# Optimization experiments

Measured on AMD Instinct MI355X. Metric: run time of the kernel, lower is better.

Reference implementation:

```python
import jax, jax.numpy as jnp
import numpy as np

D = 256
FF = 1024
NH = 8
BZ, TL = 8, 1024
L, Hs, Ws = 1, 64, 64


def _linear(x, w, b):
    # torch nn.Linear convention: w is [out, in]
    return x @ w.T + b


def _ln(x, g, b, eps=1e-5):
    m = x.mean(-1, keepdims=True)
    v = ((x - m) ** 2).mean(-1, keepdims=True)
    return (x - m) / jnp.sqrt(v + eps) * g + b


def setup_inputs() -> dict:
    key = jax.random.key(0)
    ks = jax.random.split(key, 16)
    s = 0.02
    inp = {
        "tgt": jax.random.normal(ks[0], (BZ, TL, D), jnp.float32),
        "reference_points": jax.random.uniform(ks[1], (BZ, TL, 2), jnp.float32),
        "srcs": jax.random.normal(ks[2], (BZ, L, D, Hs, Ws), jnp.float32),
        "posemb_2d": jax.random.normal(ks[3], (BZ, TL, D), jnp.float32),
        # self-attn (nn.MultiheadAttention) params
        "in_proj_w": jax.random.normal(ks[4], (3 * D, D), jnp.float32) * s,
        "in_proj_b": jnp.zeros((3 * D,), jnp.float32),
        "out_proj_w": jax.random.normal(ks[5], (D, D), jnp.float32) * s,
        "out_proj_b": jnp.zeros((D,), jnp.float32),
        # hand-rolled cross-attn linears (q, k, v, out)
        "lin_q_w": jax.random.normal(ks[6], (D, D), jnp.float32) * s,
        "lin_q_b": jnp.zeros((D,), jnp.float32),
        "lin_k_w": jax.random.normal(ks[7], (D, D), jnp.float32) * s,
        "lin_k_b": jnp.zeros((D,), jnp.float32),
        "lin_v_w": jax.random.normal(ks[8], (D, D), jnp.float32) * s,
        "lin_v_b": jnp.zeros((D,), jnp.float32),
        "lin_o_w": jax.random.normal(ks[9], (D, D), jnp.float32) * s,
        "lin_o_b": jnp.zeros((D,), jnp.float32),
        # layer norms
        "norm1_g": jnp.ones((D,), jnp.float32),
        "norm1_b": jnp.zeros((D,), jnp.float32),
        "norm2_g": jnp.ones((D,), jnp.float32),
        "norm2_b": jnp.zeros((D,), jnp.float32),
        # FFN
        "ffn_w1": jax.random.normal(ks[10], (FF, D), jnp.float32) * s,
        "ffn_b1": jnp.zeros((FF,), jnp.float32),
        "ffn_w2": jax.random.normal(ks[11], (D, FF), jnp.float32) * s,
        "ffn_b2": jnp.zeros((D,), jnp.float32),
        "ffn_norm_g": jnp.ones((D,), jnp.float32),
        "ffn_norm_b": jnp.zeros((D,), jnp.float32),
    }
    return inp


def reference(tgt, reference_points, srcs, posemb_2d,
              in_proj_w, in_proj_b, out_proj_w, out_proj_b,
              lin_q_w, lin_q_b, lin_k_w, lin_k_b, lin_v_w, lin_v_b,
              lin_o_w, lin_o_b,
              norm1_g, norm1_b, norm2_g, norm2_b,
              ffn_w1, ffn_b1, ffn_w2, ffn_b2, ffn_norm_g, ffn_norm_b):
    bz, tl, c = tgt.shape
    nh = NH
    dh = c // nh
    scale = dh ** -0.5

    # ---- self-attention (nn.MultiheadAttention math) ----
    qk = tgt + posemb_2d  # q = k = with_pos_embed(tgt, posemb_2d_)
    wq, wk, wv = in_proj_w[:c], in_proj_w[c:2 * c], in_proj_w[2 * c:]
    bq, bk, bv = in_proj_b[:c], in_proj_b[c:2 * c], in_proj_b[2 * c:]
    qp = _linear(qk, wq, bq).reshape(bz, tl, nh, dh)
    kp = _linear(qk, wk, bk).reshape(bz, tl, nh, dh)
    vp = _linear(tgt, wv, bv).reshape(bz, tl, nh, dh)
    att = jax.nn.softmax(jnp.einsum('bqhd,bkhd->bhqk', qp * scale, kp), axis=-1)
    sa = jnp.einsum('bhqk,bkhd->bqhd', att, vp).reshape(bz, tl, c)
    sa = _linear(sa, out_proj_w, out_proj_b)
    tgt = _ln(tgt + sa, norm2_g, norm2_b)

    # ---- hand-rolled cross attention ----
    bz_, l, c_, h, w = srcs.shape
    s = jnp.transpose(srcs.reshape(bz_ * l, c_, h, w), (0, 2, 3, 1)).reshape(bz_ * l, h * w, c_)
    query = _linear(tgt, lin_q_w, lin_q_b)          # [bz, tl, c]
    key = _linear(s, lin_k_w, lin_k_b)              # [bz*l, hw, c]
    value = _linear(s, lin_v_w, lin_v_b)
    affinity = jax.nn.softmax(jnp.einsum('bqc,bkc->bqk', query, key), axis=-1)  # no 1/sqrt(d) scale, faithful
    tgt2 = _linear(jnp.einsum('bqk,bkc->bqc', affinity, value), lin_o_w, lin_o_b)
    tgt = _ln(tgt + tgt2, norm1_g, norm1_b)

    # ---- FFN ----
    src2 = _linear(jax.nn.relu(_linear(tgt, ffn_w1, ffn_b1)), ffn_w2, ffn_b2)
    tgt = _ln(tgt + src2, ffn_norm_g, ffn_norm_b)
    return tgt
```

## Files before the change

### kernel.cpp

```cpp
#include <hip/hip_runtime.h>
#include <hip/hip_bf16.h>
#include <math.h>

typedef __attribute__((ext_vector_type(8))) __bf16 bf16x8;
typedef __attribute__((ext_vector_type(4))) __bf16 bf16x4;
typedef __attribute__((ext_vector_type(2))) __bf16 bf16x2;
typedef __attribute__((ext_vector_type(4))) float  f32x4;

#define MFMA16(a,b,c) __builtin_amdgcn_mfma_f32_16x16x32_bf16((a),(b),(c),0,0,0)

__device__ __forceinline__ unsigned pack2bf(float a, float b){
  bf16x2 t; t[0] = (__bf16)a; t[1] = (__bf16)b;
  return __builtin_bit_cast(unsigned, t);
}
__device__ __forceinline__ int perm1(int r){ return ((r<<2)|(r>>1)) & 7; }

template<int BM, bool RELU, int OUTMODE, bool ADD2>
__global__ __launch_bounds__(256) void gemm_bt(
    const float* __restrict__ A, const float* __restrict__ A2,
    const float* __restrict__ W,
    const float* __restrict__ bias, void* __restrict__ Cv,
    int M, int N, int K, int ldc, int coff, float oscale)
{
  constexpr int MT = BM/32;
  __shared__ __align__(16) __bf16 As[BM][40];
  __shared__ __align__(16) __bf16 Bs[64][40];

  const int tid  = threadIdx.x;
  const int wid  = tid >> 6;
  const int lane = tid & 63;
  const int wr   = wid >> 1;
  const int wc   = wid & 1;
  const int lq   = lane & 15;
  const int lk8  = (lane >> 4) << 3;
  const int rb   = (lane >> 4) << 2;

  const int m0 = blockIdx.x * BM;
  const int n0 = blockIdx.y * 64;

  const int scg = (tid & 7) << 2;
  const int sr  = tid >> 3;

  f32x4 acc[MT][2];
  #pragma unroll
  for (int i=0;i<MT;i++)
    #pragma unroll
    for (int j=0;j<2;j++) acc[i][j] = f32x4{0.f,0.f,0.f,0.f};

  for (int k0=0; k0<K; k0+=32){
    __syncthreads();
    #pragma unroll
    for (int i=0;i<MT;i++){
      const int row = sr + i*32;
      float4 a4 = *(const float4*)&A[(size_t)(m0+row)*K + k0 + scg];
      if (ADD2){
        const float4 a42 = *(const float4*)&A2[(size_t)(m0+row)*K + k0 + scg];
        a4.x+=a42.x; a4.y+=a42.y; a4.z+=a42.z; a4.w+=a42.w;
      }
      bf16x4 h; h[0]=(__bf16)a4.x; h[1]=(__bf16)a4.y; h[2]=(__bf16)a4.z; h[3]=(__bf16)a4.w;
      *(bf16x4*)&As[row][scg] = h;
    }
    #pragma unroll
    for (int i=0;i<2;i++){
      const int row = sr + i*32;
      const float4 a4 = *(const float4*)&W[(size_t)(n0+row)*K + k0 + scg];
      bf16x4 h; h[0]=(__bf16)a4.x; h[1]=(__bf16)a4.y; h[2]=(__bf16)a4.z; h[3]=(__bf16)a4.w;
      *(bf16x4*)&Bs[row][scg] = h;
    }
    __syncthreads();
    bf16x8 af[MT], bfr[2];
    #pragma unroll
    for (int i=0;i<MT;i++) af[i]  = *(const bf16x8*)&As[wr*(BM/2) + i*16 + lq][lk8];
    #pragma unroll
    for (int j=0;j<2;j++)  bfr[j] = *(const bf16x8*)&Bs[wc*32 + j*16 + lq][lk8];
    #pragma unroll
    for (int i=0;i<MT;i++)
      #pragma unroll
      for (int j=0;j<2;j++)
        acc[i][j] = MFMA16(af[i], bfr[j], acc[i][j]);
  }

  #pragma unroll
  for (int i=0;i<MT;i++)
    #pragma unroll
    for (int j=0;j<2;j++){
      const int coln = n0 + wc*32 + j*16 + lq;
      const float bv = bias ? bias[coln] : 0.f;
      if (OUTMODE == 2){
        const int rowm0 = m0 + wr*(BM/2) + i*16 + rb;
        bf16x4 hv;
        #pragma unroll
        for (int r=0;r<4;r++){
          float vv = (acc[i][j][r] + bv) * oscale;
          if (RELU) vv = fmaxf(vv, 0.f);
          hv[r] = (__bf16)vv;
        }
        *(bf16x4*)&((__bf16*)Cv)[((size_t)((rowm0>>10)*256) + coln)*1024 + (rowm0&1023)] = hv;
      } else {
        #pragma unroll
        for (int r=0;r<4;r++){
          const int rowm = m0 + wr*(BM/2) + i*16 + rb + r;
          float vv = (acc[i][j][r] + bv) * oscale;
          if (RELU) vv = fmaxf(vv, 0.f);
          const size_t idx = (size_t)rowm*ldc + coff + coln;
          if (OUTMODE == 1) ((__bf16*)Cv)[idx] = (__bf16)vv;
          else              ((float*)Cv)[idx]  = vv;
        }
      }
    }
}

template<bool TRANSOUT>
__global__ __launch_bounds__(256) void gemm_srcs(
    const float* __restrict__ S, const float* __restrict__ W,
    const float* __restrict__ bias, __bf16* __restrict__ C)
{
  __shared__ __align__(16) __bf16 As[128][40];
  __shared__ __align__(16) __bf16 Bs[64][40];

  const int tid  = threadIdx.x;
  const int wid  = tid >> 6;
  const int lane = tid & 63;
  const int wr   = wid >> 1;
  const int wc   = wid & 1;
  const int lq   = lane & 15;
  const int lk8  = (lane >> 4) << 3;
  const int rb   = (lane >> 4) << 2;

  const int m0 = blockIdx.x * 128;
  const int n0 = blockIdx.y * 64;
  const int bb = m0 >> 12;
  const int p0 = m0 & 4095;

  const int cA = tid & 31;
  const int qA = tid >> 5;
  const int scg = (tid & 7) << 2;
  const int sr  = tid >> 3;

  f32x4 acc[4][2];
  #pragma unroll
  for (int i=0;i<4;i++)
    #pragma unroll
    for (int j=0;j<2;j++) acc[i][j] = f32x4{0.f,0.f,0.f,0.f};

  for (int k0=0; k0<256; k0+=32){
    __syncthreads();
    const float* sbase = &S[((size_t)bb*256 + k0 + cA)*4096 + p0];
    #pragma unroll
    for (int ps=0; ps<4; ps++){
      const int p = ps*32 + qA*4;
      const float4 f4 = *(const float4*)(sbase + p);
      As[p+0][cA] = (__bf16)f4.x;
      As[p+1][cA] = (__bf16)f4.y;
      As[p+2][cA] = (__bf16)f4.z;
      As[p+3][cA] = (__bf16)f4.w;
    }
    #pragma unroll
    for (int i=0;i<2;i++){
      const int row = sr + i*32;
      const float4 a4 = *(const float4*)&W[(size_t)(n0+row)*256 + k0 + scg];
      bf16x4 h; h[0]=(__bf16)a4.x; h[1]=(__bf16)a4.y; h[2]=(__bf16)a4.z; h[3]=(__bf16)a4.w;
      *(bf16x4*)&Bs[row][scg] = h;
    }
    __syncthreads();
    bf16x8 af[4], bfr[2];
    #pragma unroll
    for (int i=0;i<4;i++) af[i]  = *(const bf16x8*)&As[wr*64 + i*16 + lq][lk8];
    #pragma unroll
    for (int j=0;j<2;j++) bfr[j] = *(const bf16x8*)&Bs[wc*32 + j*16 + lq][lk8];
    #pragma unroll
    for (int i=0;i<4;i++)
      #pragma unroll
      for (int j=0;j<2;j++)
        acc[i][j] = MFMA16(af[i], bfr[j], acc[i][j]);
  }

  #pragma unroll
  for (int i=0;i<4;i++)
    #pragma unroll
    for (int j=0;j<2;j++){
      const int coln = n0 + wc*32 + j*16 + lq;
      const float bv = bias ? bias[coln] : 0.f;
      if (TRANSOUT){
        bf16x4 hv;
        #pragma unroll
        for (int r=0;r<4;r++) hv[r] = (__bf16)(acc[i][j][r] + bv);
        *(bf16x4*)&C[((size_t)bb*256 + coln)*4096 + p0 + wr*64 + i*16 + rb] = hv;
      } else {
        #pragma unroll
        for (int r=0;r<4;r++){
          const int rowm = m0 + wr*64 + i*16 + rb + r;
          C[(size_t)rowm*256 + coln] = (__bf16)(acc[i][j][r] + bv);
        }
      }
    }
}

__global__ __launch_bounds__(256) void ln_kernel(const float* __restrict__ res,
                                                 const float* __restrict__ x,
                                                 const float* __restrict__ g,
                                                 const float* __restrict__ beta,
                                                 float* __restrict__ out)
{
  const int row  = blockIdx.x*4 + (threadIdx.x >> 6);
  const int lane = threadIdx.x & 63;
  const int c = lane*4;
  const float4 rv = *(const float4*)&res[(size_t)row*256 + c];
  const float4 xv = *(const float4*)&x[(size_t)row*256 + c];
  float v0=rv.x+xv.x, v1=rv.y+xv.y, v2=rv.z+xv.z, v3=rv.w+xv.w;
  float s = v0+v1+v2+v3;
  #pragma unroll
  for (int off=1; off<64; off<<=1) s += __shfl_xor(s, off);
  const float mean = s * (1.f/256.f);
  const float d0=v0-mean, d1=v1-mean, d2=v2-mean, d3=v3-mean;
  float q = d0*d0 + d1*d1 + d2*d2 + d3*d3;
  #pragma unroll
  for (int off=1; off<64; off<<=1) q += __shfl_xor(q, off);
  const float rstd = rsqrtf(q*(1.f/256.f) + 1e-5f);
  const float4 gv = *(const float4*)&g[c];
  const float4 bv = *(const float4*)&beta[c];
  float4 ov;
  ov.x = d0*rstd*gv.x + bv.x;
  ov.y = d1*rstd*gv.y + bv.y;
  ov.z = d2*rstd*gv.z + bv.z;
  ov.w = d3*rstd*gv.w + bv.w;
  *(float4*)&out[(size_t)row*256 + c] = ov;
}

__global__ __launch_bounds__(256) void flash_self(
    const __bf16* __restrict__ qs, const __bf16* __restrict__ ks,
    const __bf16* __restrict__ vts, float* __restrict__ sa)
{
  const int qt = blockIdx.x;
  const int b  = blockIdx.y >> 3;
  const int h  = blockIdx.y & 7;
  const int tid  = threadIdx.x;
  const int wid  = tid >> 6;
  const int lane = tid & 63;
  const int lq   = lane & 15;
  const int hi   = lane >> 4;
  const int lk8  = hi << 3;
  const int rb   = hi << 2;

  const int qrow = b*1024 + qt*64 + wid*16 + lq;
  const bf16x8 qf = *(const bf16x8*)&qs[(size_t)qrow*256 + h*32 + lk8];

  const __bf16* kb0 = &ks[(size_t)(b*1024 + lq)*256 + h*32 + lk8];
  const __bf16* vb0 = &vts[(size_t)(b*256 + h*32 + lq)*1024 + lk8];

  const f32x4 Z = {0.f, 0.f, 0.f, 0.f};
  float m = -1e30f, l = 0.f;
  f32x4 o0 = Z, o1 = Z;

  for (int it=0; it<16; ++it){
    const int key0 = it*64;
    f32x4 s4[4];
    #pragma unroll
    for (int kt=0;kt<4;kt++){
      const bf16x8 kf = *(const bf16x8*)(kb0 + (size_t)(key0 + kt*16)*256);
      s4[kt] = MFMA16(kf, qf, Z);
    }
    float pm = s4[0][0];
    #pragma unroll
    for (int kt=0;kt<4;kt++)
      #pragma unroll
      for (int r=0;r<4;r++) pm = fmaxf(pm, s4[kt][r]);
    pm = fmaxf(pm, __shfl_xor(pm,16));
    pm = fmaxf(pm, __shfl_xor(pm,32));
    if (!__all(pm <= m + 8.f)){
      const float mn = fmaxf(m, pm);
      const float alpha = __expf(m - mn);
      o0[0]*=alpha; o0[1]*=alpha; o0[2]*=alpha; o0[3]*=alpha;
      o1[0]*=alpha; o1[1]*=alpha; o1[2]*=alpha; o1[3]*=alpha;
      l *= alpha;
      m = mn;
    }
    float p[4][4]; float rs = 0.f;
    #pragma unroll
    for (int kt=0;kt<4;kt++)
      #pragma unroll
      for (int r=0;r<4;r++){ p[kt][r] = __expf(s4[kt][r]-m); rs += p[kt][r]; }
    rs += __shfl_xor(rs,16);
    rs += __shfl_xor(rs,32);
    l += rs;
    unsigned pk0[4], pk1[4];
    #pragma unroll
    for (int kt=0;kt<4;kt++){
      pk0[kt] = pack2bf(p[kt][0], p[kt][1]);
      pk1[kt] = pack2bf(p[kt][2], p[kt][3]);
    }
    const int srcA = ((hi&1)<<5) + lq;
    const int srcB = srcA + 16;
    const bool ksel = hi >= 2;
    bf16x8 pf[2];
    #pragma unroll
    for (int ks2=0; ks2<2; ks2++){
      const unsigned a0 = (unsigned)__shfl((int)pk0[2*ks2],   srcA);
      const unsigned a1 = (unsigned)__shfl((int)pk0[2*ks2+1], srcA);
      const unsigned b0 = (unsigned)__shfl((int)pk1[2*ks2],   srcA);
      const unsigned b1 = (unsigned)__shfl((int)pk1[2*ks2+1], srcA);
      const unsigned c0 = (unsigned)__shfl((int)pk0[2*ks2],   srcB);
      const unsigned c1 = (unsigned)__shfl((int)pk0[2*ks2+1], srcB);
      const unsigned d0 = (unsigned)__shfl((int)pk1[2*ks2],   srcB);
      const unsigned d1 = (unsigned)__shfl((int)pk1[2*ks2+1], srcB);
      union { unsigned u[4]; bf16x8 v; } uu;
      uu.u[0] = ksel ? a1 : a0;
      uu.u[1] = ksel ? b1 : b0;
      uu.u[2] = ksel ? c1 : c0;
      uu.u[3] = ksel ? d1 : d0;
      pf[ks2] = uu.v;
    }
    #pragma unroll
    for (int ks2=0; ks2<2; ks2++){
      const bf16x8 vf0 = *(const bf16x8*)(vb0 + key0 + ks2*32);
      const bf16x8 vf1 = *(const bf16x8*)(vb0 + (size_t)16*1024 + key0 + ks2*32);
      o0 = MFMA16(vf0, pf[ks2], o0);
      o1 = MFMA16(vf1, pf[ks2], o1);
    }
  }
  const float inv = 1.f / l;
  f32x4 w0, w1;
  #pragma unroll
  for (int r=0;r<4;r++){ w0[r] = o0[r]*inv; w1[r] = o1[r]*inv; }
  *(f32x4*)&sa[(size_t)qrow*256 + h*32 + rb]      = w0;
  *(f32x4*)&sa[(size_t)qrow*256 + h*32 + 16 + rb] = w1;
}

__global__ __launch_bounds__(256, 1) void flash_cross(
    const __bf16* __restrict__ qgm, const __bf16* __restrict__ kg,
    const __bf16* __restrict__ vtg, __bf16* __restrict__ Opart,
    float* __restrict__ ml)
{
  extern __shared__ __bf16 smem[];
  __bf16* Ks = smem;
  __bf16* Vt = smem + 64*256;

  const int bid = blockIdx.x;
  const int xcd = bid & 7;
  const int grp = bid >> 3;
  const int qt  = grp & 7;
  const int pp  = xcd + 8*(grp >> 3);
  const int b   = pp >> 3;
  const int sl  = pp & 7;

  const int tid  = threadIdx.x;
  const int wid  = tid >> 6;
  const int lane = tid & 63;
  const int lq   = lane & 15;
  const int hi   = lane >> 4;
  const int lk8  = hi << 3;
  const int rb   = hi << 2;
  const int p1l  = perm1(lq & 7);

  const int q0 = b*1024 + qt*128 + wid*32;
  bf16x8 qf[2][8];
  #pragma unroll
  for (int g=0; g<2; g++)
    #pragma unroll
    for (int ks=0; ks<8; ks++)
      qf[g][ks] = *(const bf16x8*)&qgm[(size_t)(q0 + g*16 + lq)*256 + ks*32 + lk8];

  const f32x4 Z = {0.f, 0.f, 0.f, 0.f};
  float m[2] = {-1e30f, -1e30f};
  float l[2] = {0.f, 0.f};
  f32x4 o[2][16];
  #pragma unroll
  for (int g=0; g<2; g++)
    #pragma unroll
    for (int nf=0; nf<16; nf++) o[g][nf] = Z;

  const int srow = tid >> 2;
  const int c4   = tid & 3;
  const int p1s  = perm1(srow & 7);

  for (int it=0; it<8; ++it){
    const int key0 = sl*512 + it*64;
    __syncthreads();
    {
      const __bf16* kb = &kg[(size_t)(b*4096 + key0 + srow)*256];
      #pragma unroll
      for (int j=0;j<8;j++){
        const int ch = c4 + j*4;
        *(bf16x8*)&Ks[srow*256 + ((ch ^ p1s)<<3)] = *(const bf16x8*)(kb + ch*8);
      }
    }
    {
      #pragma unroll
      for (int ps=0; ps<4; ps++){
        const int d = srow + ps*64;
        const __bf16* vb = &vtg[(size_t)(b*256 + d)*4096 + key0];
        #pragma unroll
        for (int s2=0;s2<2;s2++){
          const int ch = c4 + s2*4;
          *(bf16x8*)&Vt[d*64 + ((ch ^ p1s)<<3)] = *(const bf16x8*)(vb + ch*8);
        }
      }
    }
    __syncthreads();
    f32x4 s4[2][4];
    #pragma unroll
    for (int g=0; g<2; g++)
      #pragma unroll
      for (int kt=0;kt<4;kt++) s4[g][kt] = Z;
    #pragma unroll
    for (int ks=0; ks<8; ks++){
      #pragma unroll
      for (int kt=0; kt<4; kt++){
        const bf16x8 kf = *(const bf16x8*)&Ks[(kt*16+lq)*256 + (((ks*4+hi) ^ p1l)<<3)];
        s4[0][kt] = MFMA16(kf, qf[0][ks], s4[0][kt]);
        s4[1][kt] = MFMA16(kf, qf[1][ks], s4[1][kt]);
      }
    }
    float pm[2];
    #pragma unroll
    for (int g=0; g<2; g++){
      float v = s4[g][0][0];
      #pragma unroll
      for (int kt=0;kt<4;kt++)
        #pragma unroll
        for (int r=0;r<4;r++) v = fmaxf(v, s4[g][kt][r]);
      v = fmaxf(v, __shfl_xor(v, 16));
      v = fmaxf(v, __shfl_xor(v, 32));
      pm[g] = v;
    }
    const bool need = (pm[0] > m[0] + 8.f) || (pm[1] > m[1] + 8.f);
    if (__any(need)){
      #pragma unroll
      for (int g=0; g<2; g++){
        const float mn = fmaxf(m[g], pm[g]);
        const float alpha = __expf(m[g] - mn);
        #pragma unroll
        for (int nf=0;nf<16;nf++){
          o[g][nf][0]*=alpha; o[g][nf][1]*=alpha;
          o[g][nf][2]*=alpha; o[g][nf][3]*=alpha;
        }
        l[g] *= alpha;
        m[g] = mn;
      }
    }
    bf16x8 pf[2][2];
    #pragma unroll
    for (int g=0; g<2; g++){
      float p[4][4];
      float rs = 0.f;
      #pragma unroll
      for (int kt=0;kt<4;kt++)
        #pragma unroll
        for (int r=0;r<4;r++){ p[kt][r] = __expf(s4[g][kt][r] - m[g]); rs += p[kt][r]; }
      rs += __shfl_xor(rs, 16);
      rs += __shfl_xor(rs, 32);
      l[g] += rs;
      unsigned pk0[4], pk1[4];
      #pragma unroll
      for (int kt=0;kt<4;kt++){
        pk0[kt] = pack2bf(p[kt][0], p[kt][1]);
        pk1[kt] = pack2bf(p[kt][2], p[kt][3]);
      }
      const int srcA = ((hi&1)<<5) + lq;
      const int srcB = srcA + 16;
      const bool ksel = hi >= 2;
      #pragma unroll
      for (int ks2=0; ks2<2; ks2++){
        const unsigned a0 = (unsigned)__shfl((int)pk0[2*ks2],   srcA);
        const unsigned a1 = (unsigned)__shfl((int)pk0[2*ks2+1], srcA);
        const unsigned b0 = (unsigned)__shfl((int)pk1[2*ks2],   srcA);
        const unsigned b1 = (unsigned)__shfl((int)pk1[2*ks2+1], srcA);
        const unsigned c0 = (unsigned)__shfl((int)pk0[2*ks2],   srcB);
        const unsigned c1 = (unsigned)__shfl((int)pk0[2*ks2+1], srcB);
        const unsigned d0 = (unsigned)__shfl((int)pk1[2*ks2],   srcB);
        const unsigned d1 = (unsigned)__shfl((int)pk1[2*ks2+1], srcB);
        union { unsigned u[4]; bf16x8 v; } uu;
        uu.u[0] = ksel ? a1 : a0;
        uu.u[1] = ksel ? b1 : b0;
        uu.u[2] = ksel ? c1 : c0;
        uu.u[3] = ksel ? d1 : d0;
        pf[g][ks2] = uu.v;
      }
    }
    #pragma unroll
    for (int nf=0; nf<16; nf++){
      #pragma unroll
      for (int ks2=0; ks2<2; ks2++){
        const bf16x8 af = *(const bf16x8*)&Vt[(nf*16+lq)*64 + (((ks2*4+hi) ^ p1l)<<3)];
        o[0][nf] = MFMA16(af, pf[0][ks2], o[0][nf]);
        o[1][nf] = MFMA16(af, pf[1][ks2], o[1][nf]);
      }
    }
  }
  #pragma unroll
  for (int g=0; g<2; g++){
    const int row = q0 + g*16 + lq;
    if (hi == 0){
      ml[(size_t)(sl*8192 + row)*2 + 0] = m[g];
      ml[(size_t)(sl*8192 + row)*2 + 1] = l[g];
    }
    #pragma unroll
    for (int nf=0; nf<16; nf++){
      bf16x4 hv;
      #pragma unroll
      for (int r=0;r<4;r++) hv[r] = (__bf16)o[g][nf][r];
      *(bf16x4*)&Opart[(size_t)(sl*8192 + row)*256 + nf*16 + rb] = hv;
    }
  }
}

__global__ __launch_bounds__(256) void combine_kernel(const __bf16* __restrict__ Opart,
                                                      const float* __restrict__ ml,
                                                      float* __restrict__ out)
{
  const int row = blockIdx.x;
  const int d = threadIdx.x;
  float mm[8], ll[8];
  #pragma unroll
  for (int s=0;s<8;s++){
    mm[s] = ml[(size_t)(s*8192+row)*2 + 0];
    ll[s] = ml[(size_t)(s*8192+row)*2 + 1];
  }
  float M = mm[0];
  #pragma unroll
  for (int s=1;s<8;s++) M = fmaxf(M, mm[s]);
  float L = 0.f, acc = 0.f;
  #pragma unroll
  for (int s=0;s<8;s++){
    const float e = __expf(mm[s]-M);
    L   += ll[s]*e;
    acc += e * (float)Opart[(size_t)(s*8192+row)*256 + d];
  }
  out[(size_t)row*256 + d] = acc / L;
}

extern "C" void kernel_launch(void* const* d_in, const int* in_sizes, int n_in,
                              void* d_out, int out_size, void* d_ws, size_t ws_size,
                              hipStream_t stream)
{
  (void)in_sizes; (void)n_in; (void)out_size; (void)ws_size;
  const float* tgt        = (const float*)d_in[0];
  const float* srcs       = (const float*)d_in[2];
  const float* posemb     = (const float*)d_in[3];
  const float* in_proj_w  = (const float*)d_in[4];
  const float* in_proj_b  = (const float*)d_in[5];
  const float* out_proj_w = (const float*)d_in[6];
  const float* out_proj_b = (const float*)d_in[7];
  const float* lin_q_w    = (const float*)d_in[8];
  const float* lin_q_b    = (const float*)d_in[9];
  const float* lin_k_w    = (const float*)d_in[10];
  const float* lin_k_b    = (const float*)d_in[11];
  const float* lin_v_w    = (const float*)d_in[12];
  const float* lin_v_b    = (const float*)d_in[13];
  const float* lin_o_w    = (const float*)d_in[14];
  const float* lin_o_b    = (const float*)d_in[15];
  const float* norm1_g    = (const float*)d_in[16];
  const float* norm1_b    = (const float*)d_in[17];
  const float* norm2_g    = (const float*)d_in[18];
  const float* norm2_b    = (const float*)d_in[19];
  const float* ffn_w1     = (const float*)d_in[20];
  const float* ffn_b1     = (const float*)d_in[21];
  const float* ffn_w2     = (const float*)d_in[22];
  const float* ffn_b2     = (const float*)d_in[23];
  const float* ffn_norm_g = (const float*)d_in[24];
  const float* ffn_norm_b = (const float*)d_in[25];
  float* out = (float*)d_out;

  char* w = (char*)d_ws;
  const size_t MB = (size_t)1 << 20;
  float*  tgt1    = (float*)(w + 0);
  float*  sa      = (float*)(w + 8*MB);
  __bf16* query_b = (__bf16*)(w + 8*MB);
  float*  attn2   = (float*)(w + 8*MB);
  float*  ffn_out = (float*)(w + 8*MB);
  __bf16* q_s     = (__bf16*)(w + 16*MB);
  __bf16* key_b   = (__bf16*)(w + 16*MB);
  float*  t2proj  = (float*)(w + 16*MB);
  __bf16* k_s     = (__bf16*)(w + 20*MB);
  __bf16* v_t     = (__bf16*)(w + 24*MB);
  float*  tgt3    = (float*)(w + 24*MB);
  float*  saproj  = (float*)(w + 28*MB);
  __bf16* val_t   = (__bf16*)(w + 32*MB);
  float*  ffn_h   = (float*)(w + 32*MB);
  __bf16* Opart   = (__bf16*)(w + 48*MB);
  float*  ml      = (float*)(w + 80*MB);

  const float SCALE = 0.17677669529663687f;

  gemm_bt<64,false,1,true><<<dim3(128,4),256,0,stream>>>(tgt, posemb,
      in_proj_w, in_proj_b, q_s, 8192,256,256, 256,0, SCALE);
  gemm_bt<64,false,1,true><<<dim3(128,4),256,0,stream>>>(tgt, posemb,
      in_proj_w + 256*256, in_proj_b + 256, k_s, 8192,256,256, 256,0, 1.f);
  gemm_bt<64,false,2,false><<<dim3(128,4),256,0,stream>>>(tgt, nullptr,
      in_proj_w + 512*256, in_proj_b + 512, v_t, 8192,256,256, 256,0, 1.f);
  flash_self<<<dim3(16,64),256,0,stream>>>(q_s, k_s, v_t, sa);
  gemm_bt<64,false,0,false><<<dim3(128,4),256,0,stream>>>(sa, nullptr,
      out_proj_w, out_proj_b, saproj, 8192,256,256, 256,0, 1.f);
  ln_kernel<<<2048,256,0,stream>>>(tgt, saproj, norm2_g, norm2_b, tgt1);

  gemm_bt<64,false,1,false><<<dim3(128,4),256,0,stream>>>(tgt1, nullptr,
      lin_q_w, lin_q_b, query_b, 8192,256,256, 256,0, 1.f);
  gemm_srcs<false><<<dim3(256,4),256,0,stream>>>(srcs, lin_k_w, lin_k_b, key_b);
  gemm_srcs<true ><<<dim3(256,4),256,0,stream>>>(srcs, lin_v_w, lin_v_b, val_t);
  flash_cross<<<512,256,65536,stream>>>(query_b, key_b, val_t, Opart, ml);
  combine_kernel<<<8192,256,0,stream>>>(Opart, ml, attn2);
  gemm_bt<64,false,0,false><<<dim3(128,4),256,0,stream>>>(attn2, nullptr,
      lin_o_w, lin_o_b, t2proj, 8192,256,256, 256,0, 1.f);
  ln_kernel<<<2048,256,0,stream>>>(tgt1, t2proj, norm1_g, norm1_b, tgt3);

  gemm_bt<128,true,0,false><<<dim3(64,16),256,0,stream>>>(tgt3, nullptr,
      ffn_w1, ffn_b1, ffn_h, 8192,1024,256, 1024,0, 1.f);
  gemm_bt<64,false,0,false><<<dim3(128,4),256,0,stream>>>(ffn_h, nullptr,
      ffn_w2, ffn_b2, ffn_out, 8192,256,1024, 256,0, 1.f);
  ln_kernel<<<2048,256,0,stream>>>(tgt3, ffn_out, ffn_norm_g, ffn_norm_b, out);
}
```

Baseline: 308.5 us.

## Use bf16 intermediates, fuse Q/K projection, and widen GEMM K-tile to 64

Intermediate activations (self-attention output, cross-attention combine output, LN outputs, FFN hidden) are now written in bf16 and consumed directly by GEMMs through a new AMODE=2 path. This roughly halves memory traffic for those buffers. The Q and K in-projections are merged into one GEMM producing an interleaved 512-wide buffer, and the softmax scale moves into flash_self. The GEMM K-step grows from 32 to 64 with wider per-thread loads, which raises LDS use and register pressure.

```diff
diff --git a/kernel.cpp b/kernel.cpp
--- a/kernel.cpp
+++ b/kernel.cpp
@@ -15,16 +15,24 @@
 }
 __device__ __forceinline__ int perm1(int r){ return ((r<<2)|(r>>1)) & 7; }
 
-template<int BM, bool RELU, int OUTMODE, bool ADD2>
+__device__ __forceinline__ bf16x8 cvt8(const float4& a, const float4& b){
+  bf16x8 h;
+  h[0]=(__bf16)a.x; h[1]=(__bf16)a.y; h[2]=(__bf16)a.z; h[3]=(__bf16)a.w;
+  h[4]=(__bf16)b.x; h[5]=(__bf16)b.y; h[6]=(__bf16)b.z; h[7]=(__bf16)b.w;
+  return h;
+}
+
+template<int BM, bool RELU, int OUTMODE, int AMODE>
 __global__ __launch_bounds__(256) void gemm_bt(
-    const float* __restrict__ A, const float* __restrict__ A2,
+    const void* __restrict__ Av, const float* __restrict__ A2,
     const float* __restrict__ W,
     const float* __restrict__ bias, void* __restrict__ Cv,
     int M, int N, int K, int ldc, int coff, float oscale)
 {
   constexpr int MT = BM/32;
-  __shared__ __align__(16) __bf16 As[BM][40];
-  __shared__ __align__(16) __bf16 Bs[64][40];
+  constexpr int PASSES = BM/64;
+  __shared__ __align__(16) __bf16 As[BM][72];
+  __shared__ __align__(16) __bf16 Bs[64][72];
 
   const int tid  = threadIdx.x;
   const int wid  = tid >> 6;
@@ -38,8 +46,8 @@
   const int m0 = blockIdx.x * BM;
   const int n0 = blockIdx.y * 64;
 
-  const int scg = (tid & 7) << 2;
-  const int sr  = tid >> 3;
+  const int sr = tid >> 2;
+  const int sc = (tid & 3) << 4;
 
   f32x4 acc[MT][2];
   #pragma unroll
@@ -47,37 +55,59 @@
     #pragma unroll
     for (int j=0;j<2;j++) acc[i][j] = f32x4{0.f,0.f,0.f,0.f};
 
-  for (int k0=0; k0<K; k0+=32){
+  for (int k0=0; k0<K; k0+=64){
     __syncthreads();
     #pragma unroll
-    for (int i=0;i<MT;i++){
-      const int row = sr + i*32;
-      float4 a4 = *(const float4*)&A[(size_t)(m0+row)*K + k0 + scg];
-      if (ADD2){
-        const float4 a42 = *(const float4*)&A2[(size_t)(m0+row)*K + k0 + scg];
-        a4.x+=a42.x; a4.y+=a42.y; a4.z+=a42.z; a4.w+=a42.w;
-      }
-      bf16x4 h; h[0]=(__bf16)a4.x; h[1]=(__bf16)a4.y; h[2]=(__bf16)a4.z; h[3]=(__bf16)a4.w;
-      *(bf16x4*)&As[row][scg] = h;
-    }
-    #pragma unroll
-    for (int i=0;i<2;i++){
-      const int row = sr + i*32;
-      const float4 a4 = *(const float4*)&W[(size_t)(n0+row)*K + k0 + scg];
-      bf16x4 h; h[0]=(__bf16)a4.x; h[1]=(__bf16)a4.y; h[2]=(__bf16)a4.z; h[3]=(__bf16)a4.w;
-      *(bf16x4*)&Bs[row][scg] = h;
+    for (int p=0;p<PASSES;p++){
+      const int row = sr + p*64;
+      if (AMODE == 2){
+        const __bf16* ap = (const __bf16*)Av + (size_t)(m0+row)*K + k0 + sc;
+        *(bf16x8*)&As[row][sc]   = *(const bf16x8*)(ap);
+        *(bf16x8*)&As[row][sc+8] = *(const bf16x8*)(ap + 8);
+      } else {
+        const float* ap = (const float*)Av + (size_t)(m0+row)*K + k0 + sc;
+        float4 a0 = *(const float4*)(ap);
+        float4 a1 = *(const float4*)(ap+4);
+        float4 a2 = *(const float4*)(ap+8);
+        float4 a3 = *(const float4*)(ap+12);
+        if (AMODE == 1){
+          const float* bp = A2 + (size_t)(m0+row)*K + k0 + sc;
+          const float4 b0 = *(const float4*)(bp);
+          const float4 b1 = *(const float4*)(bp+4);
+          const float4 b2 = *(const float4*)(bp+8);
+          const float4 b3 = *(const float4*)(bp+12);
+          a0.x+=b0.x; a0.y+=b0.y; a0.z+=b0.z; a0.w+=b0.w;
+          a1.x+=b1.x; a1.y+=b1.y; a1.z+=b1.z; a1.w+=b1.w;
+          a2.x+=b2.x; a2.y+=b2.y; a2.z+=b2.z; a2.w+=b2.w;
+          a3.x+=b3.x; a3.y+=b3.y; a3.z+=b3.z; a3.w+=b3.w;
+        }
+        *(bf16x8*)&As[row][sc]   = cvt8(a0,a1);
+        *(bf16x8*)&As[row][sc+8] = cvt8(a2,a3);
+      }
+    }
+    {
+      const float* wp = W + (size_t)(n0+sr)*K + k0 + sc;
+      const float4 a0 = *(const float4*)(wp);
+      const float4 a1 = *(const float4*)(wp+4);
+      const float4 a2 = *(const float4*)(wp+8);
+      const float4 a3 = *(const float4*)(wp+12);
+      *(bf16x8*)&Bs[sr][sc]   = cvt8(a0,a1);
+      *(bf16x8*)&Bs[sr][sc+8] = cvt8(a2,a3);
     }
     __syncthreads();
-    bf16x8 af[MT], bfr[2];
-    #pragma unroll
-    for (int i=0;i<MT;i++) af[i]  = *(const bf16x8*)&As[wr*(BM/2) + i*16 + lq][lk8];
-    #pragma unroll
-    for (int j=0;j<2;j++)  bfr[j] = *(const bf16x8*)&Bs[wc*32 + j*16 + lq][lk8];
-    #pragma unroll
-    for (int i=0;i<MT;i++)
+    #pragma unroll
+    for (int ksub=0; ksub<2; ksub++){
+      bf16x8 bfr[2];
       #pragma unroll
       for (int j=0;j<2;j++)
-        acc[i][j] = MFMA16(af[i], bfr[j], acc[i][j]);
+        bfr[j] = *(const bf16x8*)&Bs[wc*32 + j*16 + lq][ksub*32 + lk8];
+      #pragma unroll
+      for (int i=0;i<MT;i++){
+        const bf16x8 af = *(const bf16x8*)&As[wr*(BM/2) + i*16 + lq][ksub*32 + lk8];
+        acc[i][0] = MFMA16(af, bfr[0], acc[i][0]);
+        acc[i][1] = MFMA16(af, bfr[1], acc[i][1]);
+      }
+    }
   }
 
   #pragma unroll
@@ -200,7 +230,8 @@
                                                  const float* __restrict__ x,
                                                  const float* __restrict__ g,
                                                  const float* __restrict__ beta,
-                                                 float* __restrict__ out)
+                                                 float* __restrict__ out,
+                                                 __bf16* __restrict__ outb)
 {
   const int row  = blockIdx.x*4 + (threadIdx.x >> 6);
   const int lane = threadIdx.x & 63;
@@ -225,11 +256,16 @@
   ov.z = d2*rstd*gv.z + bv.z;
   ov.w = d3*rstd*gv.w + bv.w;
   *(float4*)&out[(size_t)row*256 + c] = ov;
+  if (outb){
+    bf16x4 hv;
+    hv[0]=(__bf16)ov.x; hv[1]=(__bf16)ov.y; hv[2]=(__bf16)ov.z; hv[3]=(__bf16)ov.w;
+    *(bf16x4*)&outb[(size_t)row*256 + c] = hv;
+  }
 }
 
 __global__ __launch_bounds__(256) void flash_self(
-    const __bf16* __restrict__ qs, const __bf16* __restrict__ ks,
-    const __bf16* __restrict__ vts, float* __restrict__ sa)
+    const __bf16* __restrict__ qks, const __bf16* __restrict__ vts,
+    __bf16* __restrict__ sab)
 {
   const int qt = blockIdx.x;
   const int b  = blockIdx.y >> 3;
@@ -241,11 +277,12 @@
   const int hi   = lane >> 4;
   const int lk8  = hi << 3;
   const int rb   = hi << 2;
+  const float SCALE = 0.17677669529663687f;
 
   const int qrow = b*1024 + qt*64 + wid*16 + lq;
-  const bf16x8 qf = *(const bf16x8*)&qs[(size_t)qrow*256 + h*32 + lk8];
-
-  const __bf16* kb0 = &ks[(size_t)(b*1024 + lq)*256 + h*32 + lk8];
+  const bf16x8 qf = *(const bf16x8*)&qks[(size_t)qrow*512 + h*32 + lk8];
+
+  const __bf16* kb0 = &qks[(size_t)(b*1024 + lq)*512 + 256 + h*32 + lk8];
   const __bf16* vb0 = &vts[(size_t)(b*256 + h*32 + lq)*1024 + lk8];
 
   const f32x4 Z = {0.f, 0.f, 0.f, 0.f};
@@ -257,8 +294,10 @@
     f32x4 s4[4];
     #pragma unroll
     for (int kt=0;kt<4;kt++){
-      const bf16x8 kf = *(const bf16x8*)(kb0 + (size_t)(key0 + kt*16)*256);
+      const bf16x8 kf = *(const bf16x8*)(kb0 + (size_t)(key0 + kt*16)*512);
       s4[kt] = MFMA16(kf, qf, Z);
+      #pragma unroll
+      for (int r=0;r<4;r++) s4[kt][r] *= SCALE;
     }
     float pm = s4[0][0];
     #pragma unroll
@@ -319,11 +358,11 @@
     }
   }
   const float inv = 1.f / l;
-  f32x4 w0, w1;
-  #pragma unroll
-  for (int r=0;r<4;r++){ w0[r] = o0[r]*inv; w1[r] = o1[r]*inv; }
-  *(f32x4*)&sa[(size_t)qrow*256 + h*32 + rb]      = w0;
-  *(f32x4*)&sa[(size_t)qrow*256 + h*32 + 16 + rb] = w1;
+  bf16x4 w0, w1;
+  #pragma unroll
+  for (int r=0;r<4;r++){ w0[r] = (__bf16)(o0[r]*inv); w1[r] = (__bf16)(o1[r]*inv); }
+  *(bf16x4*)&sab[(size_t)qrow*256 + h*32 + rb]      = w0;
+  *(bf16x4*)&sab[(size_t)qrow*256 + h*32 + 16 + rb] = w1;
 }
 
 __global__ __launch_bounds__(256, 1) void flash_cross(
@@ -506,7 +545,7 @@
 
 __global__ __launch_bounds__(256) void combine_kernel(const __bf16* __restrict__ Opart,
                                                       const float* __restrict__ ml,
-                                                      float* __restrict__ out)
+                                                      __bf16* __restrict__ out)
 {
   const int row = blockIdx.x;
   const int d = threadIdx.x;
@@ -526,7 +565,7 @@
     L   += ll[s]*e;
     acc += e * (float)Opart[(size_t)(s*8192+row)*256 + d];
   }
-  out[(size_t)row*256 + d] = acc / L;
+  out[(size_t)row*256 + d] = (__bf16)(acc / L);
 }
 
 extern "C" void kernel_launch(void* const* d_in, const int* in_sizes, int n_in,
@@ -564,48 +603,45 @@
   char* w = (char*)d_ws;
   const size_t MB = (size_t)1 << 20;
   float*  tgt1    = (float*)(w + 0);
-  float*  sa      = (float*)(w + 8*MB);
+  __bf16* qk_s    = (__bf16*)(w + 8*MB);
   __bf16* query_b = (__bf16*)(w + 8*MB);
-  float*  attn2   = (float*)(w + 8*MB);
-  float*  ffn_out = (float*)(w + 8*MB);
-  __bf16* q_s     = (__bf16*)(w + 16*MB);
+  __bf16* tgt1b   = (__bf16*)(w + 12*MB);
+  __bf16* attn2   = (__bf16*)(w + 12*MB);
+  __bf16* v_t     = (__bf16*)(w + 16*MB);
   __bf16* key_b   = (__bf16*)(w + 16*MB);
   float*  t2proj  = (float*)(w + 16*MB);
-  __bf16* k_s     = (__bf16*)(w + 20*MB);
-  __bf16* v_t     = (__bf16*)(w + 24*MB);
+  __bf16* sa_b    = (__bf16*)(w + 20*MB);
+  float*  saproj  = (float*)(w + 24*MB);
   float*  tgt3    = (float*)(w + 24*MB);
-  float*  saproj  = (float*)(w + 28*MB);
   __bf16* val_t   = (__bf16*)(w + 32*MB);
-  float*  ffn_h   = (float*)(w + 32*MB);
+  __bf16* ffn_h   = (__bf16*)(w + 32*MB);
   __bf16* Opart   = (__bf16*)(w + 48*MB);
+  float*  ffn_out = (float*)(w + 48*MB);
+  __bf16* tgt3b   = (__bf16*)(w + 56*MB);
   float*  ml      = (float*)(w + 80*MB);
 
-  const float SCALE = 0.17677669529663687f;
-
-  gemm_bt<64,false,1,true><<<dim3(128,4),256,0,stream>>>(tgt, posemb,
-      in_proj_w, in_proj_b, q_s, 8192,256,256, 256,0, SCALE);
-  gemm_bt<64,false,1,true><<<dim3(128,4),256,0,stream>>>(tgt, posemb,
-      in_proj_w + 256*256, in_proj_b + 256, k_s, 8192,256,256, 256,0, 1.f);
-  gemm_bt<64,false,2,false><<<dim3(128,4),256,0,stream>>>(tgt, nullptr,
+  gemm_bt<64,false,1,1><<<dim3(128,8),256,0,stream>>>(tgt, posemb,
+      in_proj_w, in_proj_b, qk_s, 8192,512,256, 512,0, 1.f);
+  gemm_bt<64,false,2,0><<<dim3(128,4),256,0,stream>>>(tgt, nullptr,
       in_proj_w + 512*256, in_proj_b + 512, v_t, 8192,256,256, 256,0, 1.f);
-  flash_self<<<dim3(16,64),256,0,stream>>>(q_s, k_s, v_t, sa);
-  gemm_bt<64,false,0,false><<<dim3(128,4),256,0,stream>>>(sa, nullptr,
+  flash_self<<<dim3(16,64),256,0,stream>>>(qk_s, v_t, sa_b);
+  gemm_bt<64,false,0,2><<<dim3(128,4),256,0,stream>>>(sa_b, nullptr,
       out_proj_w, out_proj_b, saproj, 8192,256,256, 256,0, 1.f);
-  ln_kernel<<<2048,256,0,stream>>>(tgt, saproj, norm2_g, norm2_b, tgt1);
-
-  gemm_bt<64,false,1,false><<<dim3(128,4),256,0,stream>>>(tgt1, nullptr,
+  ln_kernel<<<2048,256,0,stream>>>(tgt, saproj, norm2_g, norm2_b, tgt1, tgt1b);
+
+  gemm_bt<64,false,1,2><<<dim3(128,4),256,0,stream>>>(tgt1b, nullptr,
       lin_q_w, lin_q_b, query_b, 8192,256,256, 256,0, 1.f);
   gemm_srcs<false><<<dim3(256,4),256,0,stream>>>(srcs, lin_k_w, lin_k_b, key_b);
   gemm_srcs<true ><<<dim3(256,4),256,0,stream>>>(srcs, lin_v_w, lin_v_b, val_t);
   flash_cross<<<512,256,65536,stream>>>(query_b, key_b, val_t, Opart, ml);
   combine_kernel<<<8192,256,0,stream>>>(Opart, ml, attn2);
-  gemm_bt<64,false,0,false><<<dim3(128,4),256,0,stream>>>(attn2, nullptr,
+  gemm_bt<64,false,0,2><<<dim3(128,4),256,0,stream>>>(attn2, nullptr,
       lin_o_w, lin_o_b, t2proj, 8192,256,256, 256,0, 1.f);
-  ln_kernel<<<2048,256,0,stream>>>(tgt1, t2proj, norm1_g, norm1_b, tgt3);
-
-  gemm_bt<128,true,0,false><<<dim3(64,16),256,0,stream>>>(tgt3, nullptr,
+  ln_kernel<<<2048,256,0,stream>>>(tgt1, t2proj, norm1_g, norm1_b, tgt3, tgt3b);
+
+  gemm_bt<128,true,1,2><<<dim3(64,16),256,0,stream>>>(tgt3b, nullptr,
       ffn_w1, ffn_b1, ffn_h, 8192,1024,256, 1024,0, 1.f);
-  gemm_bt<64,false,0,false><<<dim3(128,4),256,0,stream>>>(ffn_h, nullptr,
+  gemm_bt<64,false,0,2><<<dim3(128,4),256,0,stream>>>(ffn_h, nullptr,
       ffn_w2, ffn_b2, ffn_out, 8192,256,1024, 256,0, 1.f);
-  ln_kernel<<<2048,256,0,stream>>>(tgt3, ffn_out, ffn_norm_g, ffn_norm_b, out);
-}
+  ln_kernel<<<2048,256,0,stream>>>(tgt3, ffn_out, ffn_norm_g, ffn_norm_b, out, nullptr);
+}
```

Result: faster. 293.3 us (-4.9%).
